# Kernel tuning notes

Measured on AMD Instinct MI355X. Metric: run time of the kernel, lower is better.

## Reference

```python
import jax, jax.numpy as jnp
import numpy as np

N, T, D = 32, 64, 16
F = 512  # object_classes == feature dim after object_fc


def _gcn(x, adj, W, b):
    # Kipf GraphConvolution: adj @ (x @ W) + b
    return adj @ (x @ W) + b


def _norm_adj(a):
    d = jnp.sum(a, axis=1) ** -0.5
    return a * d[:, None] * d[None, :]


def _per_graph(x, gc1_W, gc1_b, gc2_W, gc2_b, gc3_W, gc3_b, gc4_W, gc4_b):
    # x: [D, F]
    # graph_generator / adj2: softmax-style similarity adjacency with D^{-1/2} norm
    s = x @ x.T                                   # [D, D]
    a = jnp.exp(s - jnp.max(s, axis=1, keepdims=True))
    adj = _norm_adj(a)
    # branch 1
    x1 = jax.nn.relu(_gcn(x, adj, gc1_W, gc1_b))
    x1 = _gcn(x1, adj, gc2_W, gc2_b)
    # branch 2 (adj_hat2 identical construction from x)
    y2 = jax.nn.relu(_gcn(x, adj, gc3_W, gc3_b))  # [D, 32]
    y22 = y2 @ y2.T
    nrm = jnp.sqrt(jnp.sum(y22 * y22, axis=1, keepdims=True))  # torch.norm(y22, 2, dim=1)
    adj3 = 1.0 + y22 / (nrm @ nrm.T)
    adj_hat3 = _norm_adj(adj3)
    y2 = _gcn(y2, adj_hat3, gc4_W, gc4_b)
    return (x1 + y2) * 0.5


def setup_inputs() -> dict:
    key = jax.random.key(0)
    ks = jax.random.split(key, 12)
    s = 0.02
    return {
        "object_raw": jax.random.normal(ks[0], (N * T * D, F), jnp.float32),
        "action_raw": jax.random.normal(ks[1], (N * T, F), jnp.float32),
        "W_obj": jax.random.normal(ks[2], (F, 512), jnp.float32) * s,
        "b_obj": jnp.zeros((512,), jnp.float32),
        "W_act": jax.random.normal(ks[3], (F, 512), jnp.float32) * s,
        "b_act": jnp.zeros((512,), jnp.float32),
        "gc1_W": jax.random.normal(ks[4], (512, 32), jnp.float32) * s,
        "gc1_b": jnp.zeros((32,), jnp.float32),
        "gc2_W": jax.random.normal(ks[5], (32, 512), jnp.float32) * s,
        "gc2_b": jnp.zeros((512,), jnp.float32),
        "gc3_W": jax.random.normal(ks[6], (512, 32), jnp.float32) * s,
        "gc3_b": jnp.zeros((32,), jnp.float32),
        "gc4_W": jax.random.normal(ks[7], (32, 512), jnp.float32) * s,
        "gc4_b": jnp.zeros((512,), jnp.float32),
        "fc1_W": jax.random.normal(ks[8], (512, 1024), jnp.float32) * s,
        "fc1_b": jnp.zeros((1024,), jnp.float32),
        "clf_W": jax.random.normal(ks[9], (1024, 500), jnp.float32) * s,
        "clf_b": jnp.zeros((500,), jnp.float32),
    }


def reference(object_raw, action_raw, W_obj, b_obj, W_act, b_act,
              gc1_W, gc1_b, gc2_W, gc2_b, gc3_W, gc3_b, gc4_W, gc4_b,
              fc1_W, fc1_b, clf_W, clf_b):
    obj = jax.nn.relu(object_raw @ W_obj + b_obj).reshape(N * T, D, 512)
    act = jax.nn.relu(action_raw @ W_act + b_act)           # [N*T, 512]
    obj = obj.at[:, D // 2].set(act)                         # overwrite middle frame
    graph = jax.vmap(lambda x: _per_graph(x, gc1_W, gc1_b, gc2_W, gc2_b,
                                          gc3_W, gc3_b, gc4_W, gc4_b))(obj)
    g = graph.reshape(N, T, D, 512).mean(axis=2)
    o = obj.reshape(N, T, D, 512).mean(axis=2)
    feat = (o + g) * 0.5                                     # graph_fusion == 'mean'
    c = jax.nn.relu(feat)                                    # dropout = identity (eval)
    c = jax.nn.relu(c @ fc1_W + fc1_b)
    out = (c @ clf_W + clf_b).mean(axis=1)                   # mean over T -> [N, 500]
    return out
```

## Files before the change

kernel.cpp:

```cpp
#include <hip/hip_runtime.h>
#include <hip/hip_bf16.h>

using ushort_t = unsigned short;
using f32x4  = __attribute__((ext_vector_type(4))) float;
using short8 = __attribute__((ext_vector_type(8))) short;

__device__ __forceinline__ float bflo(unsigned p) {
    union { unsigned u; float f; } x; x.u = p << 16; return x.f;
}
__device__ __forceinline__ float bfhi(unsigned p) {
    union { unsigned u; float f; } x; x.u = p & 0xffff0000u; return x.f;
}
__device__ __forceinline__ ushort_t f2bf(float f) {
    __hip_bfloat16 h = __float2bfloat16(f);
    return *(ushort_t*)&h;
}
__device__ __forceinline__ unsigned pk2bf(float lo, float hi) {
    __hip_bfloat162 h = __float22bfloat162_rn({lo, hi});
    return *(unsigned*)&h;
}

__device__ __forceinline__ void tr_tile(const float* __restrict__ S, ushort_t* __restrict__ D,
                                        int K, int N, int Npad, int bx, int by,
                                        int tx, int ty, float* tile )
{
    const int k0 = by * 32, n0 = bx * 32;
#pragma unroll
    for (int r = 0; r < 4; r++) {
        const int k = k0 + ty + r * 8, n = n0 + tx;
        tile[(ty + r * 8) * 33 + tx] = (k < K && n < N) ? S[(size_t)k * N + n] : 0.f;
    }
    __syncthreads();
#pragma unroll
    for (int r = 0; r < 4; r++) {
        const int n = n0 + ty + r * 8, k = k0 + tx;
        if (n < Npad && k < K) D[(size_t)n * K + k] = f2bf(tile[tx * 33 + ty + r * 8]);
    }
}

__device__ __forceinline__ void trf_tile(const float* __restrict__ S, float* __restrict__ D,
                                         int K, int N, int bx, int by,
                                         int tx, int ty, float* tile )
{
    const int k0 = by * 32, n0 = bx * 32;
#pragma unroll
    for (int r = 0; r < 4; r++) {
        const int k = k0 + ty + r * 8, n = n0 + tx;
        tile[(ty + r * 8) * 33 + tx] = (k < K && n < N) ? S[(size_t)k * N + n] : 0.f;
    }
    __syncthreads();
#pragma unroll
    for (int r = 0; r < 4; r++) {
        const int n = n0 + ty + r * 8, k = k0 + tx;
        if (n < N && k < K) D[(size_t)n * K + k] = tile[tx * 33 + ty + r * 8];
    }
}

__global__ __launch_bounds__(256)
void prep_weights(const float* __restrict__ Wobj, ushort_t* __restrict__ WobjT,
                  const float* __restrict__ Wact, ushort_t* __restrict__ WactT,
                  const float* __restrict__ fc1W, ushort_t* __restrict__ fc1T,
                  const float* __restrict__ gc1W, ushort_t* __restrict__ W1t,
                  const float* __restrict__ gc3W, ushort_t* __restrict__ W3t,
                  const float* __restrict__ gc2W, ushort_t* __restrict__ W2bf,
                  const float* __restrict__ gc4W, ushort_t* __restrict__ W4bf,
                  const float* __restrict__ clfW, float* __restrict__ WclfT)
{
    __shared__ float tile[32 * 33];
    const int b = blockIdx.x;
    const int t = threadIdx.x;
    const int tx = t & 31, ty = t >> 5;

    if (b < 1056) {
        const float* S; ushort_t* D; int K, N, Npad, nt, l;
        if      (b < 256)  { S = Wobj; D = WobjT; K = 512; N = 512;  Npad = 512;  nt = 16; l = b; }
        else if (b < 512)  { S = Wact; D = WactT; K = 512; N = 512;  Npad = 512;  nt = 16; l = b - 256; }
        else if (b < 1024) { S = fc1W; D = fc1T;  K = 512; N = 1024; Npad = 1024; nt = 32; l = b - 512; }
        else if (b < 1040) { S = gc1W; D = W1t;   K = 512; N = 32;   Npad = 32;   nt = 1;  l = b - 1024; }
        else               { S = gc3W; D = W3t;   K = 512; N = 32;   Npad = 32;   nt = 1;  l = b - 1040; }
        tr_tile(S, D, K, N, Npad, l % nt, l / nt, tx, ty, tile);
    } else if (b < 1072) {
        const float* S = (b < 1064) ? gc2W : gc4W;
        ushort_t* D    = (b < 1064) ? W2bf : W4bf;
        const int i = (b < 1064 ? b - 1056 : b - 1064) * 256 + t;
        const float4 x = ((const float4*)S)[2 * i];
        const float4 y = ((const float4*)S)[2 * i + 1];
        unsigned r[4] = { pk2bf(x.x, x.y), pk2bf(x.z, x.w), pk2bf(y.x, y.y), pk2bf(y.z, y.w) };
        ((uint4*)D)[i] = *(uint4*)r;
    } else {
        const int l = b - 1072;
        trf_tile(clfW, WclfT, 1024, 500, l & 15, l >> 4, tx, ty, tile);
    }
}

typedef __attribute__((address_space(1))) void glb_void;
typedef __attribute__((address_space(3))) void lds_void;
__device__ __forceinline__ void dma16(const void* g, void* l) {
    __builtin_amdgcn_global_load_lds((glb_void*)(unsigned long long)(uintptr_t)g,
                                     (lds_void*)(unsigned)(uintptr_t)l, 16, 0, 0);
}

template<int RELU, typename AT>
__global__ __launch_bounds__(256)
void gemm_dma(const AT* __restrict__ A, const ushort_t* __restrict__ Bt,
              const float* __restrict__ bias, ushort_t* __restrict__ C,
              int N, int K, int Nb, int row_mul, int row_add)
{
    __shared__ __align__(16) char     AsRaw[128 * 32 * sizeof(AT)];
    __shared__ __align__(16) ushort_t Bs[128 * 32];
    const int t = threadIdx.x;
    const int lane = t & 63, w = t >> 6;
    const int bm = blockIdx.y * 128, bn = blockIdx.x * 128;
    const int mb = (w & 1) * 64, nb = (w >> 1) * 64;
    const int fr = lane & 15, fq = lane >> 4;

    f32x4 acc[16];
#pragma unroll
    for (int i = 0; i < 16; i++) acc[i] = (f32x4){0.f, 0.f, 0.f, 0.f};

    const int brow = lane >> 2, bk = lane & 3;
    const int klog = bk ^ ((brow >> 1) & 3);
    const int arow = lane >> 3, ag = lane & 7;

    for (int k0 = 0; k0 < K; k0 += 32) {
        __syncthreads();
        if constexpr (sizeof(AT) == 4) {
#pragma unroll
            for (int i = 0; i < 4; i++) {
                const int grp = w * 4 + i;
                const int row = grp * 8 + arow;
                const int gl = ag ^ (row & 7);
                dma16((const float*)A + (size_t)(bm + row) * K + k0 + gl * 4,
                      AsRaw + grp * 1024);
            }
        } else {
#pragma unroll
            for (int i = 0; i < 2; i++) {
                const int grp = w * 2 + i;
                const int row = grp * 16 + brow;
                dma16((const ushort_t*)A + (size_t)(bm + row) * K + k0 + klog * 8,
                      (ushort_t*)AsRaw + grp * 512);
            }
        }
#pragma unroll
        for (int i = 0; i < 2; i++) {
            const int grp = w * 2 + i;
            const int row = grp * 16 + brow;
            dma16(Bt + (size_t)(bn + row) * K + k0 + klog * 8, Bs + grp * 512);
        }
        __syncthreads();

        short8 af[4], bf[4];
        if constexpr (sizeof(AT) == 4) {
#pragma unroll
            for (int i = 0; i < 4; i++) {
                const int row = mb + i * 16 + fr;
                const float* base = (const float*)AsRaw + row * 32;
                const f32x4 p0 = *(const f32x4*)(base + (((2 * fq)     ^ (fr & 7)) * 4));
                const f32x4 p1 = *(const f32x4*)(base + (((2 * fq + 1) ^ (fr & 7)) * 4));
                unsigned rr[4] = { pk2bf(p0.x, p0.y), pk2bf(p0.z, p0.w),
                                   pk2bf(p1.x, p1.y), pk2bf(p1.z, p1.w) };
                af[i] = *(short8*)rr;
            }
        } else {
#pragma unroll
            for (int i = 0; i < 4; i++) {
                const int row = mb + i * 16 + fr;
                af[i] = *(const short8*)((const ushort_t*)AsRaw + row * 32 + (fq ^ ((fr >> 1) & 3)) * 8);
            }
        }
#pragma unroll
        for (int j = 0; j < 4; j++) {
            const int row = nb + j * 16 + fr;
            bf[j] = *(const short8*)(Bs + row * 32 + (fq ^ ((fr >> 1) & 3)) * 8);
        }
#pragma unroll
        for (int i = 0; i < 4; i++)
#pragma unroll
            for (int j = 0; j < 4; j++)
                acc[i * 4 + j] = __builtin_amdgcn_mfma_f32_16x16x32_bf16(
                    af[i], bf[j], acc[i * 4 + j], 0, 0, 0);
    }

#pragma unroll
    for (int j = 0; j < 4; j++) {
        const int n = bn + nb + j * 16 + fr;
        const float bv = (n < Nb) ? bias[n] : 0.f;
#pragma unroll
        for (int i = 0; i < 4; i++) {
            const f32x4 a = acc[i * 4 + j];
#pragma unroll
            for (int r = 0; r < 4; r++) {
                const int m = bm + mb + i * 16 + fq * 4 + r;
                float v = a[r] + bv;
                if (RELU) v = fmaxf(v, 0.f);
                C[((size_t)m * row_mul + row_add) * (size_t)N + n] = f2bf(v);
            }
        }
    }
}

__global__ __launch_bounds__(256)
void gemm_fc1_mean(const ushort_t* __restrict__ A, const ushort_t* __restrict__ Bt,
                   const float* __restrict__ bias, float* __restrict__ cmean)
{
    __shared__ __align__(16) ushort_t AsS[128 * 32];
    __shared__ __align__(16) ushort_t Bs[128 * 32];
    const int t = threadIdx.x;
    const int lane = t & 63, w = t >> 6;
    const int bm = blockIdx.y * 128, bn = blockIdx.x * 128;
    const int mb = (w & 1) * 64, nb = (w >> 1) * 64;
    const int fr = lane & 15, fq = lane >> 4;
    const int K = 512;

    f32x4 acc[16];
#pragma unroll
    for (int i = 0; i < 16; i++) acc[i] = (f32x4){0.f, 0.f, 0.f, 0.f};

    const int brow = lane >> 2, bk = lane & 3;
    const int klog = bk ^ ((brow >> 1) & 3);

    for (int k0 = 0; k0 < K; k0 += 32) {
        __syncthreads();
#pragma unroll
        for (int i = 0; i < 2; i++) {
            const int grp = w * 2 + i;
            const int row = grp * 16 + brow;
            dma16(A + (size_t)(bm + row) * K + k0 + klog * 8, AsS + grp * 512);
        }
#pragma unroll
        for (int i = 0; i < 2; i++) {
            const int grp = w * 2 + i;
            const int row = grp * 16 + brow;
            dma16(Bt + (size_t)(bn + row) * K + k0 + klog * 8, Bs + grp * 512);
        }
        __syncthreads();

        short8 af[4], bf[4];
#pragma unroll
        for (int i = 0; i < 4; i++) {
            const int row = mb + i * 16 + fr;
            af[i] = *(const short8*)(AsS + row * 32 + (fq ^ ((fr >> 1) & 3)) * 8);
        }
#pragma unroll
        for (int j = 0; j < 4; j++) {
            const int row = nb + j * 16 + fr;
            bf[j] = *(const short8*)(Bs + row * 32 + (fq ^ ((fr >> 1) & 3)) * 8);
        }
#pragma unroll
        for (int i = 0; i < 4; i++)
#pragma unroll
            for (int j = 0; j < 4; j++)
                acc[i * 4 + j] = __builtin_amdgcn_mfma_f32_16x16x32_bf16(
                    af[i], bf[j], acc[i * 4 + j], 0, 0, 0);
    }

    const int nidx = (bm + mb) >> 6;
#pragma unroll
    for (int j = 0; j < 4; j++) {
        const int n = bn + nb + j * 16 + fr;
        const float bv = bias[n];
        float s = 0.f;
#pragma unroll
        for (int i = 0; i < 4; i++) {
            const f32x4 a = acc[i * 4 + j];
#pragma unroll
            for (int r = 0; r < 4; r++) s += fmaxf(a[r] + bv, 0.f);
        }
        s += __shfl_xor(s, 16);
        s += __shfl_xor(s, 32);
        if (fq == 0) cmean[(size_t)nidx * 1024 + n] = s * (1.0f / 64.0f);
    }
}

__global__ __launch_bounds__(512, 1)
void mega_obj_graph(const float* __restrict__ A, const ushort_t* __restrict__ Bt,
                    const float* __restrict__ bias, const ushort_t* __restrict__ act_bf,
                    const ushort_t* __restrict__ W1t, const ushort_t* __restrict__ W3t,
                    const float* __restrict__ b1, const float* __restrict__ b3,
                    const ushort_t* __restrict__ W2b, const float* __restrict__ b2,
                    const ushort_t* __restrict__ W4b, const float* __restrict__ b4,
                    ushort_t* __restrict__ cbuf)
{
    __shared__ __align__(16) ushort_t As[128 * 512];
    __shared__ __align__(16) float fsS[8][992];

    const int t = threadIdx.x;
    const int lane = t & 63, w = t >> 6;
    const int bm = blockIdx.x * 128;
    const int fr = lane & 15, fq = lane >> 4;

    const float4* A4 = (const float4*)(A + (size_t)bm * 512);
#pragma unroll
    for (int i = 0; i < 16; i++) {
        const int fl = i * 1024 + t * 2;
        const int row = fl >> 7;
        const float4 p0 = A4[fl];
        const float4 p1 = A4[fl + 1];
        unsigned rr[4] = { pk2bf(p0.x, p0.y), pk2bf(p0.z, p0.w),
                           pk2bf(p1.x, p1.y), pk2bf(p1.z, p1.w) };
        *(uint4*)&As[row * 512 + ((lane ^ (row & 7)) * 8)] = *(uint4*)rr;
    }

    const int nw = w * 64;
    const ushort_t* Bbase = Bt + (size_t)(nw + fr) * 512 + fq * 8;
    uint4 bA[4], bB[4];
#pragma unroll
    for (int j = 0; j < 4; j++) bA[j] = *(const uint4*)(Bbase + (size_t)j * 16 * 512);

    __syncthreads();

    f32x4 acc[4][8];
#pragma unroll
    for (int j = 0; j < 4; j++)
#pragma unroll
        for (int i = 0; i < 8; i++) acc[j][i] = (f32x4){0.f, 0.f, 0.f, 0.f};

    for (int kk = 0; kk < 16; kk += 2) {
        short8 af[8];
#pragma unroll
        for (int i = 0; i < 8; i++)
            af[i] = *(const short8*)&As[(i * 16 + fr) * 512 + (((kk * 4 + fq) ^ (fr & 7)) * 8)];
#pragma unroll
        for (int j = 0; j < 4; j++) {
            bB[j] = *(const uint4*)(Bbase + (size_t)j * 16 * 512 + (kk + 1) * 32);
            const short8 bf = *(const short8*)&bA[j];
#pragma unroll
            for (int i = 0; i < 8; i++)
                acc[j][i] = __builtin_amdgcn_mfma_f32_16x16x32_bf16(af[i], bf, acc[j][i], 0, 0, 0);
        }
#pragma unroll
        for (int i = 0; i < 8; i++)
            af[i] = *(const short8*)&As[(i * 16 + fr) * 512 + ((((kk + 1) * 4 + fq) ^ (fr & 7)) * 8)];
#pragma unroll
        for (int j = 0; j < 4; j++) {
            if (kk + 2 < 16)
                bA[j] = *(const uint4*)(Bbase + (size_t)j * 16 * 512 + (kk + 2) * 32);
            const short8 bf = *(const short8*)&bB[j];
#pragma unroll
            for (int i = 0; i < 8; i++)
                acc[j][i] = __builtin_amdgcn_mfma_f32_16x16x32_bf16(af[i], bf, acc[j][i], 0, 0, 0);
        }
    }

    __syncthreads();
#pragma unroll
    for (int j = 0; j < 4; j++) {
        const int col0 = nw + j * 16 + fr;
        const float bv = bias[col0];
#pragma unroll
        for (int i = 0; i < 8; i++) {
#pragma unroll
            for (int rr2 = 0; rr2 < 4; rr2++) {
                const int m = i * 16 + fq * 4 + rr2;
                As[m * 512 + ((((col0 >> 3) ^ (m & 7)) << 3) | (col0 & 7))]
                    = f2bf(fmaxf(acc[j][i][rr2] + bv, 0.f));
            }
        }
    }
    __syncthreads();

    {
        const int ra = t >> 6, gg = t & 63;
        const uint4 v = *(const uint4*)(act_bf + (size_t)(blockIdx.x * 8 + ra) * 512 + gg * 8);
        *(uint4*)&As[(ra * 16 + 8) * 512 + gg * 8] = v;
    }
    __syncthreads();

    f32x4 e0[4], e1[4];
    float om0[8], om1[8];
    const bool isT = (w == 1) || (w == 2) || (w == 5) || (w == 6);
    const int gofs = (w >= 4) ? 4 : 0;
    const int sidx = (w == 0) ? 0 : (w == 3) ? 1 : (w == 4) ? 2 : 3;
    const int gb = sidx * 2;

    if (isT) {
        const ushort_t* Wt = ((w & 3) == 1) ? W1t : W3t;
#pragma unroll
        for (int g = 0; g < 4; g++) { e0[g] = (f32x4){0.f,0.f,0.f,0.f}; e1[g] = e0[g]; }
        for (int kk = 0; kk < 16; kk++) {
            const short8 wa = *(const short8*)(Wt + (size_t)fr * 512 + kk * 32 + fq * 8);
            const short8 wb = *(const short8*)(Wt + (size_t)(16 + fr) * 512 + kk * 32 + fq * 8);
#pragma unroll
            for (int g = 0; g < 4; g++) {
                const short8 xf = *(const short8*)&As[((gofs + g) * 16 + fr) * 512 + (((kk * 4 + fq) ^ (fr & 7)) * 8)];
                e0[g] = __builtin_amdgcn_mfma_f32_16x16x32_bf16(xf, wa, e0[g], 0, 0, 0);
                e1[g] = __builtin_amdgcn_mfma_f32_16x16x32_bf16(xf, wb, e1[g], 0, 0, 0);
            }
        }
    } else {
        e0[0] = (f32x4){0.f,0.f,0.f,0.f}; e1[0] = e0[0];
        for (int kk = 0; kk < 16; kk++) {
            const short8 xf0 = *(const short8*)&As[(gb * 16 + fr) * 512 + (((kk * 4 + fq) ^ (fr & 7)) * 8)];
            const short8 xf1 = *(const short8*)&As[((gb + 1) * 16 + fr) * 512 + (((kk * 4 + fq) ^ (fr & 7)) * 8)];
            e0[0] = __builtin_amdgcn_mfma_f32_16x16x32_bf16(xf0, xf0, e0[0], 0, 0, 0);
            e1[0] = __builtin_amdgcn_mfma_f32_16x16x32_bf16(xf1, xf1, e1[0], 0, 0, 0);
        }
#pragma unroll
        for (int c = 0; c < 8; c++) { om0[c] = 0.f; om1[c] = 0.f; }
#pragma unroll
        for (int m = 0; m < 16; m++) {
            const uint4 q0 = *(const uint4*)&As[(gb * 16 + m) * 512 + ((lane ^ (m & 7)) * 8)];
            const uint4 q1 = *(const uint4*)&As[((gb + 1) * 16 + m) * 512 + ((lane ^ (m & 7)) * 8)];
            om0[0] += bflo(q0.x); om0[1] += bfhi(q0.x);
            om0[2] += bflo(q0.y); om0[3] += bfhi(q0.y);
            om0[4] += bflo(q0.z); om0[5] += bfhi(q0.z);
            om0[6] += bflo(q0.w); om0[7] += bfhi(q0.w);
            om1[0] += bflo(q1.x); om1[1] += bfhi(q1.x);
            om1[2] += bflo(q1.y); om1[3] += bfhi(q1.y);
            om1[4] += bflo(q1.z); om1[5] += bfhi(q1.z);
            om1[6] += bflo(q1.w); om1[7] += bfhi(q1.w);
        }
    }
    __syncthreads();

    float* Hs = (float*)As;
    if (isT) {
        const int toff = ((w & 3) == 1) ? 256 : 768;
#pragma unroll
        for (int g = 0; g < 4; g++) {
            float* dst = Hs + (gofs + g) * 1792 + toff;
#pragma unroll
            for (int i = 0; i < 4; i++) {
                const int m = fq * 4 + i;
                dst[m * 32 + fr]      = e0[g][i];
                dst[m * 32 + 16 + fr] = e1[g][i];
            }
        }
    } else {
        float* d0 = Hs + gb * 1792;
        float* d1 = Hs + (gb + 1) * 1792;
#pragma unroll
        for (int i = 0; i < 4; i++) {
            const int m = fq * 4 + i;
            d0[m * 16 + fr] = e0[0][i];
            d1[m * 16 + fr] = e1[0][i];
        }
        *(float4*)(d0 + 1280 + lane * 8)     = (float4){om0[0], om0[1], om0[2], om0[3]};
        *(float4*)(d0 + 1280 + lane * 8 + 4) = (float4){om0[4], om0[5], om0[6], om0[7]};
        *(float4*)(d1 + 1280 + lane * 8)     = (float4){om1[0], om1[1], om1[2], om1[3]};
        *(float4*)(d1 + 1280 + lane * 8 + 4) = (float4){om1[4], om1[5], om1[6], om1[7]};
    }
    __syncthreads();

    {
        const int r = fr, q = fq;
        const float* Hg = Hs + w * 1792;
        float* fw   = fsS[w];
        float* adjS = fw;
        float* y2S  = fw + 272;
        float* dvS  = fw + 848;
        float* cAS  = fw + 864;
        float* nrmS = fw + 880;
        float* dv3S = fw + 896;
        float* cA3S = fw + 912;
        float* zc1S = fw + 928;
        float* zc4S = fw + 960;

        const float4 sv = *(const float4*)(Hg + r * 16 + q * 4);
        float mx = fmaxf(fmaxf(sv.x, sv.y), fmaxf(sv.z, sv.w));
        mx = fmaxf(mx, __shfl_xor(mx, 16));
        mx = fmaxf(mx, __shfl_xor(mx, 32));
        const float e0s = expf(sv.x - mx), e1s = expf(sv.y - mx);
        const float e2s = expf(sv.z - mx), e3s = expf(sv.w - mx);
        float rs = e0s + e1s + e2s + e3s;
        rs += __shfl_xor(rs, 16); rs += __shfl_xor(rs, 32);
        const float dv = rsqrtf(rs);
        if (q == 0) dvS[r] = dv;
        __syncthreads();

        float ad0, ad1, ad2, ad3;
        {
            const float4 dc = *(const float4*)&dvS[q * 4];
            ad0 = e0s * dv * dc.x; ad1 = e1s * dv * dc.y;
            ad2 = e2s * dv * dc.z; ad3 = e3s * dv * dc.w;
        }
        adjS[r * 17 + q * 4 + 0] = ad0; adjS[r * 17 + q * 4 + 1] = ad1;
        adjS[r * 17 + q * 4 + 2] = ad2; adjS[r * 17 + q * 4 + 3] = ad3;
        {
            float c0s = ad0, c1s = ad1, c2s = ad2, c3s = ad3;
#pragma unroll
            for (int m = 1; m <= 8; m <<= 1) {
                c0s += __shfl_xor(c0s, m); c1s += __shfl_xor(c1s, m);
                c2s += __shfl_xor(c2s, m); c3s += __shfl_xor(c3s, m);
            }
            if (r == 0) {
                cAS[q * 4 + 0] = c0s; cAS[q * 4 + 1] = c1s;
                cAS[q * 4 + 2] = c2s; cAS[q * 4 + 3] = c3s;
            }
        }
        __syncthreads();

        const int c0 = q * 8;
        float x1v[8], y2v[8];
        {
            const float4 b1a = *(const float4*)(b1 + c0);
            const float4 b1b = *(const float4*)(b1 + c0 + 4);
            const float4 b3a = *(const float4*)(b3 + c0);
            const float4 b3b = *(const float4*)(b3 + c0 + 4);
            x1v[0]=b1a.x; x1v[1]=b1a.y; x1v[2]=b1a.z; x1v[3]=b1a.w;
            x1v[4]=b1b.x; x1v[5]=b1b.y; x1v[6]=b1b.z; x1v[7]=b1b.w;
            y2v[0]=b3a.x; y2v[1]=b3a.y; y2v[2]=b3a.z; y2v[3]=b3a.w;
            y2v[4]=b3b.x; y2v[5]=b3b.y; y2v[6]=b3b.z; y2v[7]=b3b.w;
        }
#pragma unroll
        for (int j = 0; j < 16; j++) {
            const float a = adjS[r * 17 + j];
            const float4 t1a = *(const float4*)(Hg + 256 + j * 32 + c0);
            const float4 t1b = *(const float4*)(Hg + 256 + j * 32 + c0 + 4);
            const float4 t3a = *(const float4*)(Hg + 768 + j * 32 + c0);
            const float4 t3b = *(const float4*)(Hg + 768 + j * 32 + c0 + 4);
            x1v[0] = fmaf(a, t1a.x, x1v[0]); x1v[1] = fmaf(a, t1a.y, x1v[1]);
            x1v[2] = fmaf(a, t1a.z, x1v[2]); x1v[3] = fmaf(a, t1a.w, x1v[3]);
            x1v[4] = fmaf(a, t1b.x, x1v[4]); x1v[5] = fmaf(a, t1b.y, x1v[5]);
            x1v[6] = fmaf(a, t1b.z, x1v[6]); x1v[7] = fmaf(a, t1b.w, x1v[7]);
            y2v[0] = fmaf(a, t3a.x, y2v[0]); y2v[1] = fmaf(a, t3a.y, y2v[1]);
            y2v[2] = fmaf(a, t3a.z, y2v[2]); y2v[3] = fmaf(a, t3a.w, y2v[3]);
            y2v[4] = fmaf(a, t3b.x, y2v[4]); y2v[5] = fmaf(a, t3b.y, y2v[5]);
            y2v[6] = fmaf(a, t3b.z, y2v[6]); y2v[7] = fmaf(a, t3b.w, y2v[7]);
        }
#pragma unroll
        for (int cc = 0; cc < 8; cc++) {
            x1v[cc] = fmaxf(x1v[cc], 0.f);
            y2v[cc] = fmaxf(y2v[cc], 0.f);
            y2S[r * 36 + c0 + cc] = y2v[cc];
        }
        __syncthreads();

        float yy[4] = {0.f, 0.f, 0.f, 0.f};
#pragma unroll
        for (int k4 = 0; k4 < 8; k4++) {
            const float4 yi = *(const float4*)&y2S[r * 36 + k4 * 4];
#pragma unroll
            for (int i = 0; i < 4; i++) {
                const float4 yj = *(const float4*)&y2S[(q * 4 + i) * 36 + k4 * 4];
                yy[i] = fmaf(yi.x, yj.x, yy[i]); yy[i] = fmaf(yi.y, yj.y, yy[i]);
                yy[i] = fmaf(yi.z, yj.z, yy[i]); yy[i] = fmaf(yi.w, yj.w, yy[i]);
            }
        }
        {
            float sq = 0.f;
#pragma unroll
            for (int i = 0; i < 4; i++) sq = fmaf(yy[i], yy[i], sq);
            sq += __shfl_xor(sq, 16); sq += __shfl_xor(sq, 32);
            const float nr = sqrtf(sq);
            if (q == 0) nrmS[r] = nr;
        }
        __syncthreads();

        float a3[4];
        float dv3;
        {
            const float nr = nrmS[r];
            const float4 ncv = *(const float4*)&nrmS[q * 4];
            a3[0] = 1.0f + yy[0] / (nr * ncv.x);
            a3[1] = 1.0f + yy[1] / (nr * ncv.y);
            a3[2] = 1.0f + yy[2] / (nr * ncv.z);
            a3[3] = 1.0f + yy[3] / (nr * ncv.w);
            float d3 = a3[0] + a3[1] + a3[2] + a3[3];
            d3 += __shfl_xor(d3, 16); d3 += __shfl_xor(d3, 32);
            dv3 = rsqrtf(d3);
            if (q == 0) dv3S[r] = dv3;
        }
        {
            const float cAm = cAS[r];
            float zp[8];
#pragma unroll
            for (int cc = 0; cc < 8; cc++) zp[cc] = cAm * x1v[cc];
#pragma unroll
            for (int m = 1; m <= 8; m <<= 1)
#pragma unroll
                for (int cc = 0; cc < 8; cc++) zp[cc] += __shfl_xor(zp[cc], m);
            if (r == 0)
#pragma unroll
                for (int cc = 0; cc < 8; cc++) zc1S[c0 + cc] = zp[cc];
        }
        __syncthreads();

        {
            const float4 d3c = *(const float4*)&dv3S[q * 4];
            float p0 = a3[0] * dv3 * d3c.x, p1 = a3[1] * dv3 * d3c.y;
            float p2 = a3[2] * dv3 * d3c.z, p3 = a3[3] * dv3 * d3c.w;
#pragma unroll
            for (int m = 1; m <= 8; m <<= 1) {
                p0 += __shfl_xor(p0, m); p1 += __shfl_xor(p1, m);
                p2 += __shfl_xor(p2, m); p3 += __shfl_xor(p3, m);
            }
            if (r == 0) {
                cA3S[q * 4 + 0] = p0; cA3S[q * 4 + 1] = p1;
                cA3S[q * 4 + 2] = p2; cA3S[q * 4 + 3] = p3;
            }
        }
        __syncthreads();

        {
            const float cA3m = cA3S[r];
            float zp[8];
#pragma unroll
            for (int cc = 0; cc < 8; cc++) zp[cc] = cA3m * y2v[cc];
#pragma unroll
            for (int m = 1; m <= 8; m <<= 1)
#pragma unroll
                for (int cc = 0; cc < 8; cc++) zp[cc] += __shfl_xor(zp[cc], m);
            if (r == 0)
#pragma unroll
                for (int cc = 0; cc < 8; cc++) zc4S[c0 + cc] = zp[cc];
        }
        __syncthreads();

        {
            float gm[8] = {0,0,0,0,0,0,0,0};
            const ushort_t* w2p = W2b + lane * 8;
            const ushort_t* w4p = W4b + lane * 8;
#pragma unroll 8
            for (int k = 0; k < 32; k++) {
                const float z1 = zc1S[k], z4 = zc4S[k];
                const uint4 u2 = *(const uint4*)(w2p + (size_t)k * 512);
                const uint4 u4 = *(const uint4*)(w4p + (size_t)k * 512);
                gm[0] = fmaf(z1, bflo(u2.x), gm[0]); gm[0] = fmaf(z4, bflo(u4.x), gm[0]);
                gm[1] = fmaf(z1, bfhi(u2.x), gm[1]); gm[1] = fmaf(z4, bfhi(u4.x), gm[1]);
                gm[2] = fmaf(z1, bflo(u2.y), gm[2]); gm[2] = fmaf(z4, bflo(u4.y), gm[2]);
                gm[3] = fmaf(z1, bfhi(u2.y), gm[3]); gm[3] = fmaf(z4, bfhi(u4.y), gm[3]);
                gm[4] = fmaf(z1, bflo(u2.z), gm[4]); gm[4] = fmaf(z4, bflo(u4.z), gm[4]);
                gm[5] = fmaf(z1, bfhi(u2.z), gm[5]); gm[5] = fmaf(z4, bfhi(u4.z), gm[5]);
                gm[6] = fmaf(z1, bflo(u2.w), gm[6]); gm[6] = fmaf(z4, bflo(u4.w), gm[6]);
                gm[7] = fmaf(z1, bfhi(u2.w), gm[7]); gm[7] = fmaf(z4, bfhi(u4.w), gm[7]);
            }
            const float4 oma = *(const float4*)(Hg + 1280 + lane * 8);
            const float4 omb = *(const float4*)(Hg + 1280 + lane * 8 + 4);
            const float omv[8] = {oma.x, oma.y, oma.z, oma.w, omb.x, omb.y, omb.z, omb.w};
            const float4 b2a = *(const float4*)(b2 + lane * 8);
            const float4 b2b = *(const float4*)(b2 + lane * 8 + 4);
            const float4 b4a = *(const float4*)(b4 + lane * 8);
            const float4 b4b = *(const float4*)(b4 + lane * 8 + 4);
            const float bs[8] = { b2a.x + b4a.x, b2a.y + b4a.y, b2a.z + b4a.z, b2a.w + b4a.w,
                                  b2b.x + b4b.x, b2b.y + b4b.y, b2b.z + b4b.z, b2b.w + b4b.w };
            ushort_t pk[8];
#pragma unroll
            for (int cc = 0; cc < 8; cc++) {
                const float gmean = 0.5f * bs[cc] + gm[cc] * (1.0f / 32.0f);
                const float feat  = 0.5f * (omv[cc] * 0.0625f + gmean);
                pk[cc] = f2bf(fmaxf(feat, 0.f));
            }
            *(uint4*)(cbuf + (size_t)(blockIdx.x * 8 + w) * 512 + lane * 8) = *(uint4*)pk;
        }
    }
}

__global__ __launch_bounds__(256)
void clf_col(const float* __restrict__ cmean, const float* __restrict__ Wt,
             const float* __restrict__ clf_b, float* __restrict__ out)
{
    __shared__ float red[8][33];
    const int j = blockIdx.x;
    const int t = threadIdx.x;
    const int n = t & 31, kp = t >> 5;
    const float* cm = cmean + (size_t)n * 1024 + kp * 128;
    const float* wp = Wt + (size_t)j * 1024 + kp * 128;
    float acc = 0.f;
#pragma unroll
    for (int k = 0; k < 128; k += 4) {
        const float4 c = *(const float4*)(cm + k);
        const float4 wv = *(const float4*)(wp + k);
        acc = fmaf(c.x, wv.x, acc);
        acc = fmaf(c.y, wv.y, acc);
        acc = fmaf(c.z, wv.z, acc);
        acc = fmaf(c.w, wv.w, acc);
    }
    red[kp][n] = acc;
    __syncthreads();
    if (t < 32) {
        float s = red[0][t];
#pragma unroll
        for (int p = 1; p < 8; p++) s += red[p][t];
        out[(size_t)t * 500 + j] = s + clf_b[j];
    }
}

extern "C" void kernel_launch(void* const* d_in, const int* in_sizes, int n_in,
                              void* d_out, int out_size, void* d_ws, size_t ws_size,
                              hipStream_t stream)
{
    const float* object_raw = (const float*)d_in[0];
    const float* action_raw = (const float*)d_in[1];
    const float* W_obj = (const float*)d_in[2];
    const float* b_obj = (const float*)d_in[3];
    const float* W_act = (const float*)d_in[4];
    const float* b_act = (const float*)d_in[5];
    const float* gc1_W = (const float*)d_in[6];
    const float* gc1_b = (const float*)d_in[7];
    const float* gc2_W = (const float*)d_in[8];
    const float* gc2_b = (const float*)d_in[9];
    const float* gc3_W = (const float*)d_in[10];
    const float* gc3_b = (const float*)d_in[11];
    const float* gc4_W = (const float*)d_in[12];
    const float* gc4_b = (const float*)d_in[13];
    const float* fc1_W = (const float*)d_in[14];
    const float* fc1_b = (const float*)d_in[15];
    const float* clf_W = (const float*)d_in[16];
    const float* clf_b = (const float*)d_in[17];

    char* ws = (char*)d_ws;
    const size_t MB = 1024 * 1024;
    ushort_t* act_bf = (ushort_t*)(ws);
    ushort_t* cbuf   = (ushort_t*)(ws + 2 * MB);
    float*    WclfT  = (float*)   (ws + 4 * MB);
    float*    cmean  = (float*)   (ws + 6 * MB);
    ushort_t* WobjT  = (ushort_t*)(ws + 7 * MB);
    ushort_t* WactT  = (ushort_t*)(ws + 7 * MB + 512 * 1024);
    ushort_t* fc1T   = (ushort_t*)(ws + 8 * MB);
    ushort_t* W1t    = (ushort_t*)(ws + 9 * MB);
    ushort_t* W3t    = (ushort_t*)(ws + 9 * MB + 32 * 1024);
    ushort_t* W2bf   = (ushort_t*)(ws + 9 * MB + 64 * 1024);
    ushort_t* W4bf   = (ushort_t*)(ws + 9 * MB + 96 * 1024);

    prep_weights<<<dim3(1584), 256, 0, stream>>>(
        W_obj, WobjT, W_act, WactT, fc1_W, fc1T,
        gc1_W, W1t, gc3_W, W3t, gc2_W, W2bf, gc4_W, W4bf,
        clf_W, WclfT);

    gemm_dma<1, float><<<dim3(4, 16), 256, 0, stream>>>(
        action_raw, WactT, b_act, act_bf, 512, 512, 512, 1, 0);

    mega_obj_graph<<<dim3(256), 512, 0, stream>>>(
        object_raw, WobjT, b_obj, act_bf, W1t, W3t,
        gc1_b, gc3_b, W2bf, gc2_b, W4bf, gc4_b, cbuf);

    gemm_fc1_mean<<<dim3(8, 16), 256, 0, stream>>>(cbuf, fc1T, fc1_b, cmean);

    clf_col<<<dim3(500), 256, 0, stream>>>(cmean, WclfT, clf_b, (float*)d_out);
}
```

Baseline: 217.2 us.

## Fold per-warp scratch into the As buffer and target two blocks per CU

Removes the separate fsS shared array by placing each warp's scratch (adjacency, y2, norms, column sums) inside the reused As buffer at a 4096-float stride. This lowers LDS use to 128 KB per block. The x1/y2 register arrays are now staged in LDS and reloaded later, which shortens register live ranges. Launch bounds move to 2 blocks per CU, aiming for more resident waves to hide latency, at the cost of extra LDS traffic and tighter register limits that could cause spills.

```diff
diff --git a/kernel.cpp b/kernel.cpp
--- a/kernel.cpp
+++ b/kernel.cpp
@@ -273,7 +273,7 @@
     }
 }
 
-__global__ __launch_bounds__(512, 1)
+__global__ __launch_bounds__(512, 2)
 void mega_obj_graph(const float* __restrict__ A, const ushort_t* __restrict__ Bt,
                     const float* __restrict__ bias, const ushort_t* __restrict__ act_bf,
                     const ushort_t* __restrict__ W1t, const ushort_t* __restrict__ W3t,
@@ -283,7 +283,6 @@
                     ushort_t* __restrict__ cbuf)
 {
     __shared__ __align__(16) ushort_t As[128 * 512];
-    __shared__ __align__(16) float fsS[8][992];
 
     const int t = threadIdx.x;
     const int lane = t & 63, w = t >> 6;
@@ -419,7 +418,7 @@
         const int toff = ((w & 3) == 1) ? 256 : 768;
 #pragma unroll
         for (int g = 0; g < 4; g++) {
-            float* dst = Hs + (gofs + g) * 1792 + toff;
+            float* dst = Hs + (size_t)(gofs + g) * 4096 + toff;
 #pragma unroll
             for (int i = 0; i < 4; i++) {
                 const int m = fq * 4 + i;
@@ -428,8 +427,8 @@
             }
         }
     } else {
-        float* d0 = Hs + gb * 1792;
-        float* d1 = Hs + (gb + 1) * 1792;
+        float* d0 = Hs + (size_t)gb * 4096;
+        float* d1 = Hs + (size_t)(gb + 1) * 4096;
 #pragma unroll
         for (int i = 0; i < 4; i++) {
             const int m = fq * 4 + i;
@@ -445,17 +444,17 @@
 
     {
         const int r = fr, q = fq;
-        const float* Hg = Hs + w * 1792;
-        float* fw   = fsS[w];
-        float* adjS = fw;
-        float* y2S  = fw + 272;
-        float* dvS  = fw + 848;
-        float* cAS  = fw + 864;
-        float* nrmS = fw + 880;
-        float* dv3S = fw + 896;
-        float* cA3S = fw + 912;
-        float* zc1S = fw + 928;
-        float* zc4S = fw + 960;
+        float* Hg   = Hs + (size_t)w * 4096;
+        float* x1S  = Hg + 1792;
+        float* adjS = Hg + 2304;
+        float* y2S  = Hg + 2576;
+        float* dvS  = Hg + 3152;
+        float* cAS  = Hg + 3168;
+        float* nrmS = Hg + 3184;
+        float* dv3S = Hg + 3200;
+        float* cA3S = Hg + 3216;
+        float* zc1S = Hg + 3232;
+        float* zc4S = Hg + 3264;
 
         const float4 sv = *(const float4*)(Hg + r * 16 + q * 4);
         float mx = fmaxf(fmaxf(sv.x, sv.y), fmaxf(sv.z, sv.w));
@@ -492,8 +491,8 @@
         __syncthreads();
 
         const int c0 = q * 8;
-        float x1v[8], y2v[8];
-        {
+        {
+            float x1v[8], y2v[8];
             const float4 b1a = *(const float4*)(b1 + c0);
             const float4 b1b = *(const float4*)(b1 + c0 + 4);
             const float4 b3a = *(const float4*)(b3 + c0);
@@ -502,28 +501,27 @@
             x1v[4]=b1b.x; x1v[5]=b1b.y; x1v[6]=b1b.z; x1v[7]=b1b.w;
             y2v[0]=b3a.x; y2v[1]=b3a.y; y2v[2]=b3a.z; y2v[3]=b3a.w;
             y2v[4]=b3b.x; y2v[5]=b3b.y; y2v[6]=b3b.z; y2v[7]=b3b.w;
-        }
-#pragma unroll
-        for (int j = 0; j < 16; j++) {
-            const float a = adjS[r * 17 + j];
-            const float4 t1a = *(const float4*)(Hg + 256 + j * 32 + c0);
-            const float4 t1b = *(const float4*)(Hg + 256 + j * 32 + c0 + 4);
-            const float4 t3a = *(const float4*)(Hg + 768 + j * 32 + c0);
-            const float4 t3b = *(const float4*)(Hg + 768 + j * 32 + c0 + 4);
-            x1v[0] = fmaf(a, t1a.x, x1v[0]); x1v[1] = fmaf(a, t1a.y, x1v[1]);
-            x1v[2] = fmaf(a, t1a.z, x1v[2]); x1v[3] = fmaf(a, t1a.w, x1v[3]);
-            x1v[4] = fmaf(a, t1b.x, x1v[4]); x1v[5] = fmaf(a, t1b.y, x1v[5]);
-            x1v[6] = fmaf(a, t1b.z, x1v[6]); x1v[7] = fmaf(a, t1b.w, x1v[7]);
-            y2v[0] = fmaf(a, t3a.x, y2v[0]); y2v[1] = fmaf(a, t3a.y, y2v[1]);
-            y2v[2] = fmaf(a, t3a.z, y2v[2]); y2v[3] = fmaf(a, t3a.w, y2v[3]);
-            y2v[4] = fmaf(a, t3b.x, y2v[4]); y2v[5] = fmaf(a, t3b.y, y2v[5]);
-            y2v[6] = fmaf(a, t3b.z, y2v[6]); y2v[7] = fmaf(a, t3b.w, y2v[7]);
-        }
-#pragma unroll
-        for (int cc = 0; cc < 8; cc++) {
-            x1v[cc] = fmaxf(x1v[cc], 0.f);
-            y2v[cc] = fmaxf(y2v[cc], 0.f);
-            y2S[r * 36 + c0 + cc] = y2v[cc];
+#pragma unroll
+            for (int j = 0; j < 16; j++) {
+                const float a = adjS[r * 17 + j];
+                const float4 t1a = *(const float4*)(Hg + 256 + j * 32 + c0);
+                const float4 t1b = *(const float4*)(Hg + 256 + j * 32 + c0 + 4);
+                const float4 t3a = *(const float4*)(Hg + 768 + j * 32 + c0);
+                const float4 t3b = *(const float4*)(Hg + 768 + j * 32 + c0 + 4);
+                x1v[0] = fmaf(a, t1a.x, x1v[0]); x1v[1] = fmaf(a, t1a.y, x1v[1]);
+                x1v[2] = fmaf(a, t1a.z, x1v[2]); x1v[3] = fmaf(a, t1a.w, x1v[3]);
+                x1v[4] = fmaf(a, t1b.x, x1v[4]); x1v[5] = fmaf(a, t1b.y, x1v[5]);
+                x1v[6] = fmaf(a, t1b.z, x1v[6]); x1v[7] = fmaf(a, t1b.w, x1v[7]);
+                y2v[0] = fmaf(a, t3a.x, y2v[0]); y2v[1] = fmaf(a, t3a.y, y2v[1]);
+                y2v[2] = fmaf(a, t3a.z, y2v[2]); y2v[3] = fmaf(a, t3a.w, y2v[3]);
+                y2v[4] = fmaf(a, t3b.x, y2v[4]); y2v[5] = fmaf(a, t3b.y, y2v[5]);
+                y2v[6] = fmaf(a, t3b.z, y2v[6]); y2v[7] = fmaf(a, t3b.w, y2v[7]);
+            }
+#pragma unroll
+            for (int cc = 0; cc < 8; cc++) {
+                x1S[r * 32 + c0 + cc] = fmaxf(x1v[cc], 0.f);
+                y2S[r * 36 + c0 + cc] = fmaxf(y2v[cc], 0.f);
+            }
         }
         __syncthreads();
 
@@ -564,9 +562,10 @@
         }
         {
             const float cAm = cAS[r];
-            float zp[8];
-#pragma unroll
-            for (int cc = 0; cc < 8; cc++) zp[cc] = cAm * x1v[cc];
+            const float4 xa = *(const float4*)&x1S[r * 32 + c0];
+            const float4 xb = *(const float4*)&x1S[r * 32 + c0 + 4];
+            float zp[8] = { cAm * xa.x, cAm * xa.y, cAm * xa.z, cAm * xa.w,
+                            cAm * xb.x, cAm * xb.y, cAm * xb.z, cAm * xb.w };
 #pragma unroll
             for (int m = 1; m <= 8; m <<= 1)
 #pragma unroll
@@ -595,9 +594,10 @@
 
         {
             const float cA3m = cA3S[r];
-            float zp[8];
-#pragma unroll
-            for (int cc = 0; cc < 8; cc++) zp[cc] = cA3m * y2v[cc];
+            const float4 ya = *(const float4*)&y2S[r * 36 + c0];
+            const float4 yb = *(const float4*)&y2S[r * 36 + c0 + 4];
+            float zp[8] = { cA3m * ya.x, cA3m * ya.y, cA3m * ya.z, cA3m * ya.w,
+                            cA3m * yb.x, cA3m * yb.y, cA3m * yb.z, cA3m * yb.w };
 #pragma unroll
             for (int m = 1; m <= 8; m <<= 1)
 #pragma unroll
```

Measured after the change: 217.5 us. Within noise of the previous version (+0.1%).
